# Kernel optimization log

Hardware: AMD Instinct MI355X
Metric: run time of the kernel (lower is better)

## Reference

```python
import jax, jax.numpy as jnp
import numpy as np

N_NODES = 100000
N_EDGES = 1600000
IN_DIM = 500
HID = 256
N_LAYERS = 3
N_CLASSES = 40


def setup_inputs() -> dict:
    key = jax.random.key(0)
    ks = jax.random.split(key, 16)
    x = jax.random.normal(ks[0], (N_NODES, IN_DIM), dtype=jnp.float32)
    edge_index = jax.random.randint(ks[1], (2, N_EDGES), 0, N_NODES, dtype=jnp.int64)
    s = 0.02
    embed_W = jax.random.normal(ks[2], (IN_DIM, HID), dtype=jnp.float32) * s
    embed_b = jnp.zeros((HID,), dtype=jnp.float32)
    conv_W = jax.random.normal(ks[3], (N_LAYERS, HID, HID), dtype=jnp.float32) * s
    conv_b = jnp.zeros((N_LAYERS, HID), dtype=jnp.float32)
    bn_gamma = jnp.ones((N_LAYERS, HID), dtype=jnp.float32)
    bn_beta = jnp.zeros((N_LAYERS, HID), dtype=jnp.float32)
    # classifier: 256 -> 128 -> 64 -> 32 -> 40
    cls_W0 = jax.random.normal(ks[4], (256, 128), dtype=jnp.float32) * s
    cls_b0 = jnp.zeros((128,), dtype=jnp.float32)
    cls_W1 = jax.random.normal(ks[5], (128, 64), dtype=jnp.float32) * s
    cls_b1 = jnp.zeros((64,), dtype=jnp.float32)
    cls_W2 = jax.random.normal(ks[6], (64, 32), dtype=jnp.float32) * s
    cls_b2 = jnp.zeros((32,), dtype=jnp.float32)
    cls_W3 = jax.random.normal(ks[7], (32, N_CLASSES), dtype=jnp.float32) * s
    cls_b3 = jnp.zeros((N_CLASSES,), dtype=jnp.float32)
    return dict(x=x, edge_index=edge_index, embed_W=embed_W, embed_b=embed_b,
                conv_W=conv_W, conv_b=conv_b, bn_gamma=bn_gamma, bn_beta=bn_beta,
                cls_W0=cls_W0, cls_b0=cls_b0, cls_W1=cls_W1, cls_b1=cls_b1,
                cls_W2=cls_W2, cls_b2=cls_b2, cls_W3=cls_W3, cls_b3=cls_b3)


def _gcn_forward(x, edge_index, embed_W, embed_b, conv_W, conv_b, bn_gamma, bn_beta,
                 cls_W0, cls_b0, cls_W1, cls_b1, cls_W2, cls_b2, cls_W3, cls_b3):
    src, dst = edge_index[0], edge_index[1]
    N = x.shape[0]
    # degree incl. self-loop (GCNConv add_self_loops=True)
    deg = jax.ops.segment_sum(jnp.ones_like(src, dtype=x.dtype), dst, num_segments=N) + 1.0
    dinv = jax.lax.rsqrt(deg)                       # [N]
    enorm = dinv[src] * dinv[dst]                   # [E] symmetric norm
    self_norm = (1.0 / deg)[:, None]                # [N,1] self-loop weight

    h = x @ embed_W + embed_b                       # embed; dropout is identity in eval
    for l in range(N_LAYERS):
        hw = h @ conv_W[l]                          # [N,HID] transform first
        msg = hw[src] * enorm[:, None]              # gather + normalize [E,HID]
        agg = jax.ops.segment_sum(msg, dst, num_segments=N) + hw * self_norm
        agg = agg + conv_b[l]
        hb = agg * bn_gamma[l] + bn_beta[l]         # BN eval mode (running mean 0, var 1)
        hb = jax.nn.relu(hb)
        h = hb + h                                  # residual (dims match)
    # classifier MLP
    h = jax.nn.relu(h @ cls_W0 + cls_b0)
    h = jax.nn.relu(h @ cls_W1 + cls_b1)
    h = jax.nn.relu(h @ cls_W2 + cls_b2)
    return h @ cls_W3 + cls_b3                      # logits [N, N_CLASSES]


def reference(x, edge_index, embed_W, embed_b, conv_W, conv_b, bn_gamma, bn_beta,
              cls_W0, cls_b0, cls_W1, cls_b1, cls_W2, cls_b2, cls_W3, cls_b3):
    return _gcn_forward(x, edge_index, embed_W, embed_b, conv_W, conv_b, bn_gamma, bn_beta,
                        cls_W0, cls_b0, cls_W1, cls_b1, cls_W2, cls_b2, cls_W3, cls_b3)
```

## Files before the change

kernel.cpp:

```cpp
#include <hip/hip_runtime.h>

#define N_NODES  100000
#define N_EDGES  1600000
#define IN_DIM   500
#define HID      256
#define N_LAYERS 3
#define N_CLASSES 40

typedef _Float16 f16;
typedef __attribute__((ext_vector_type(8))) _Float16 f16x8;
typedef __attribute__((ext_vector_type(4))) _Float16 f16x4;
typedef __attribute__((ext_vector_type(4))) float    f32x4;

template <int MODE>
__global__ __launch_bounds__(256) void mfma_gemm_kernel(
    const float* __restrict__ A, const f16* __restrict__ Bt,
    const float* __restrict__ bias, void* __restrict__ Cout,
    int M, int N, int K, int KP)
{
    __shared__ f16 Ah[128][32];
    __shared__ f16 Bs[128][32];

    const int tid  = threadIdx.x;
    const int lane = tid & 63;
    const int w    = tid >> 6;
    const int wr   = w >> 1;
    const int wc   = w & 1;
    const int m0   = blockIdx.x * 128;
    const int n0   = blockIdx.y * 128;

    const int srow = tid >> 2;
    const int sc8  = tid & 3;

    f32x4 acc[4][4];
    #pragma unroll
    for (int i = 0; i < 4; ++i)
        #pragma unroll
        for (int j = 0; j < 4; ++j)
            acc[i][j] = (f32x4){0.f, 0.f, 0.f, 0.f};

    for (int k0 = 0; k0 < KP; k0 += 32) {
        #pragma unroll
        for (int i = 0; i < 2; ++i) {
            const int r = srow + 64 * i;
            const int m = m0 + r;
            const int k = k0 + sc8 * 8;
            float4 lo = make_float4(0.f, 0.f, 0.f, 0.f);
            float4 hi = make_float4(0.f, 0.f, 0.f, 0.f);
            if (m < M) {
                if (k + 4 <= K) lo = *(const float4*)&A[(size_t)m * K + k];
                if (k + 8 <= K) hi = *(const float4*)&A[(size_t)m * K + k + 4];
            }
            f16x8 hv;
            hv[0] = (f16)lo.x; hv[1] = (f16)lo.y; hv[2] = (f16)lo.z; hv[3] = (f16)lo.w;
            hv[4] = (f16)hi.x; hv[5] = (f16)hi.y; hv[6] = (f16)hi.z; hv[7] = (f16)hi.w;
            *(f16x8*)&Ah[r][sc8 * 8] = hv;
        }
        #pragma unroll
        for (int i = 0; i < 2; ++i) {
            const int r = srow + 64 * i;
            *(f16x8*)&Bs[r][sc8 * 8] =
                *(const f16x8*)&Bt[(size_t)(n0 + r) * KP + k0 + sc8 * 8];
        }
        __syncthreads();

        const int fr = lane & 15;
        const int fg = (lane >> 4) * 8;
        f16x8 af[4], bf[4];
        #pragma unroll
        for (int i = 0; i < 4; ++i)
            af[i] = *(const f16x8*)&Ah[wr * 64 + i * 16 + fr][fg];
        #pragma unroll
        for (int j = 0; j < 4; ++j)
            bf[j] = *(const f16x8*)&Bs[wc * 64 + j * 16 + fr][fg];
        #pragma unroll
        for (int i = 0; i < 4; ++i)
            #pragma unroll
            for (int j = 0; j < 4; ++j)
                acc[i][j] = __builtin_amdgcn_mfma_f32_16x16x32_f16(
                    af[i], bf[j], acc[i][j], 0, 0, 0);
        __syncthreads();
    }

    const int fr = lane & 15;
    const int rg = (lane >> 4) * 4;
    #pragma unroll
    for (int i = 0; i < 4; ++i) {
        const int mrow = m0 + wr * 64 + i * 16 + rg;
        #pragma unroll
        for (int j = 0; j < 4; ++j) {
            const int col = n0 + wc * 64 + j * 16 + fr;
            const float b = (MODE == 0 || MODE == 1) ? bias[col] : 0.f;
            #pragma unroll
            for (int r = 0; r < 4; ++r) {
                const int m = mrow + r;
                if (m >= M) continue;
                float v = acc[i][j][r] + b;
                if (MODE == 1) v = fmaxf(v, 0.f);
                if (MODE == 4) ((f16*)Cout)[(size_t)m * N + col] = (f16)v;
                else           ((float*)Cout)[(size_t)m * N + col] = v;
            }
        }
    }
}

__global__ __launch_bounds__(256) void wt_kernel(
    const float* __restrict__ W, f16* __restrict__ Wt, int K, int N, int KP)
{
    const int i = blockIdx.x * 256 + threadIdx.x;
    if (i >= N * KP) return;
    const int n = i / KP;
    const int k = i - n * KP;
    Wt[i] = (k < K) ? (f16)W[(size_t)k * N + n] : (f16)0.f;
}

template <int MODE>
__global__ __launch_bounds__(256) void gemm_kernel(
    const float* __restrict__ A, const float* __restrict__ B,
    const float* __restrict__ bias, float* __restrict__ C,
    int M, int N, int K)
{
    __shared__ float As[16][68];
    __shared__ float Bsh[16][68];

    const int tid = threadIdx.x;
    const int tx = tid & 15;
    const int ty = tid >> 4;
    const int bm = blockIdx.x * 64;
    const int bn = blockIdx.y * 64;

    const int ar = tid >> 2;
    const int ac = (tid & 3) * 4;
    const int br = tid >> 4;
    const int bc = (tid & 15) * 4;

    float c[4][4] = {};

    for (int k0 = 0; k0 < K; k0 += 16) {
        {
            const int m = bm + ar;
            const int k = k0 + ac;
            float4 av = make_float4(0.f, 0.f, 0.f, 0.f);
            if (m < M && k < K) av = *(const float4*)&A[(size_t)m * K + k];
            As[ac + 0][ar] = av.x;
            As[ac + 1][ar] = av.y;
            As[ac + 2][ar] = av.z;
            As[ac + 3][ar] = av.w;
        }
        {
            const int k = k0 + br;
            const int n = bn + bc;
            float4 bv = make_float4(0.f, 0.f, 0.f, 0.f);
            if (k < K && n < N) bv = *(const float4*)&B[(size_t)k * N + n];
            Bsh[br][bc + 0] = bv.x;
            Bsh[br][bc + 1] = bv.y;
            Bsh[br][bc + 2] = bv.z;
            Bsh[br][bc + 3] = bv.w;
        }
        __syncthreads();

        #pragma unroll
        for (int kk = 0; kk < 16; ++kk) {
            const float4 av = *(const float4*)&As[kk][ty * 4];
            const float4 bv = *(const float4*)&Bsh[kk][tx * 4];
            const float a[4] = {av.x, av.y, av.z, av.w};
            const float b[4] = {bv.x, bv.y, bv.z, bv.w};
            #pragma unroll
            for (int i = 0; i < 4; ++i)
                #pragma unroll
                for (int j = 0; j < 4; ++j)
                    c[i][j] = fmaf(a[i], b[j], c[i][j]);
        }
        __syncthreads();
    }

    const int n = bn + tx * 4;
    if (n >= N) return;
    const float4 bias4 = *(const float4*)&bias[n];

    #pragma unroll
    for (int i = 0; i < 4; ++i) {
        const int m = bm + ty * 4 + i;
        if (m >= M) continue;
        float4 v = make_float4(c[i][0] + bias4.x, c[i][1] + bias4.y,
                               c[i][2] + bias4.z, c[i][3] + bias4.w);
        if (MODE == 1) {
            v.x = fmaxf(v.x, 0.f); v.y = fmaxf(v.y, 0.f);
            v.z = fmaxf(v.z, 0.f); v.w = fmaxf(v.w, 0.f);
        }
        *(float4*)&C[(size_t)m * N + n] = v;
    }
}

__global__ __launch_bounds__(256) void deg_kernel(
    const int* __restrict__ dst, int* __restrict__ deg)
{
    const int i = blockIdx.x * 256 + threadIdx.x;
    if (i < N_EDGES) atomicAdd(&deg[dst[i]], 1);
}

__global__ __launch_bounds__(256) void norm_kernel(
    const int* __restrict__ deg, float* __restrict__ dinv,
    float* __restrict__ selfnorm)
{
    const int i = blockIdx.x * 256 + threadIdx.x;
    if (i < N_NODES) {
        const float d = (float)deg[i] + 1.0f;
        dinv[i] = 1.0f / sqrtf(d);
        selfnorm[i] = 1.0f / d;
    }
}

__global__ __launch_bounds__(256) void scan1_kernel(
    const int* __restrict__ deg, int* __restrict__ offs,
    int* __restrict__ bsum, int n)
{
    __shared__ int tmp[256];
    const int i = blockIdx.x * 256 + threadIdx.x;
    const int v = (i < n) ? deg[i] : 0;
    tmp[threadIdx.x] = v;
    __syncthreads();
    #pragma unroll
    for (int off = 1; off < 256; off <<= 1) {
        const int t = (threadIdx.x >= off) ? tmp[threadIdx.x - off] : 0;
        __syncthreads();
        tmp[threadIdx.x] += t;
        __syncthreads();
    }
    const int inc = tmp[threadIdx.x];
    if (i < n) offs[i] = inc - v;
    if (threadIdx.x == 255) bsum[blockIdx.x] = inc;
}

__global__ __launch_bounds__(512) void scan2_kernel(int* __restrict__ bsum, int nb)
{
    __shared__ int tmp[512];
    const int i = threadIdx.x;
    const int v = (i < nb) ? bsum[i] : 0;
    tmp[i] = v;
    __syncthreads();
    #pragma unroll
    for (int off = 1; off < 512; off <<= 1) {
        const int t = (i >= off) ? tmp[i - off] : 0;
        __syncthreads();
        tmp[i] += t;
        __syncthreads();
    }
    if (i < nb) bsum[i] = tmp[i] - v;
}

__global__ __launch_bounds__(256) void scan3_kernel(
    int* __restrict__ offs, const int* __restrict__ bsum, int n)
{
    const int i = blockIdx.x * 256 + threadIdx.x;
    if (i < n) offs[i] += bsum[blockIdx.x];
}

__global__ __launch_bounds__(256) void fill_kernel(
    const int* __restrict__ src, const int* __restrict__ dst,
    const int* __restrict__ offs, int* __restrict__ fill,
    const float* __restrict__ dinv,
    int* __restrict__ csr_src, float* __restrict__ csr_w)
{
    const int e = blockIdx.x * 256 + threadIdx.x;
    if (e >= N_EDGES) return;
    const int s = src[e];
    const int d = dst[e];
    const int pos = offs[d] + atomicAdd(&fill[d], 1);
    csr_src[pos] = s;
    csr_w[pos] = dinv[s] * dinv[d];
}

__global__ __launch_bounds__(256) void gather_fused_kernel(
    const int* __restrict__ offs, const int* __restrict__ degi,
    const int* __restrict__ csr_src, const float* __restrict__ csr_w,
    const f16* __restrict__ hw, const float* __restrict__ snorm,
    const float* __restrict__ bias, const float* __restrict__ gamma,
    const float* __restrict__ beta, float* __restrict__ h)
{
    const int w = (blockIdx.x * 256 + threadIdx.x) >> 6;
    const int lane = threadIdx.x & 63;
    if (w >= N_NODES) return;
    const int start = offs[w];
    const int cnt = degi[w];
    const int col = lane * 4;

    float4 acc = make_float4(0.f, 0.f, 0.f, 0.f);
    int i = 0;
    for (; i + 2 <= cnt; i += 2) {
        const int   s0 = csr_src[start + i];
        const int   s1 = csr_src[start + i + 1];
        const float w0 = csr_w[start + i];
        const float w1 = csr_w[start + i + 1];
        const f16x4 v0 = *(const f16x4*)(hw + (size_t)s0 * HID + col);
        const f16x4 v1 = *(const f16x4*)(hw + (size_t)s1 * HID + col);
        acc.x = fmaf((float)v0[0], w0, acc.x); acc.y = fmaf((float)v0[1], w0, acc.y);
        acc.z = fmaf((float)v0[2], w0, acc.z); acc.w = fmaf((float)v0[3], w0, acc.w);
        acc.x = fmaf((float)v1[0], w1, acc.x); acc.y = fmaf((float)v1[1], w1, acc.y);
        acc.z = fmaf((float)v1[2], w1, acc.z); acc.w = fmaf((float)v1[3], w1, acc.w);
    }
    if (i < cnt) {
        const int   s0 = csr_src[start + i];
        const float w0 = csr_w[start + i];
        const f16x4 v0 = *(const f16x4*)(hw + (size_t)s0 * HID + col);
        acc.x = fmaf((float)v0[0], w0, acc.x); acc.y = fmaf((float)v0[1], w0, acc.y);
        acc.z = fmaf((float)v0[2], w0, acc.z); acc.w = fmaf((float)v0[3], w0, acc.w);
    }

    const float sn = snorm[w];
    const f16x4 hwv = *(const f16x4*)(hw + (size_t)w * HID + col);
    acc.x = fmaf((float)hwv[0], sn, acc.x); acc.y = fmaf((float)hwv[1], sn, acc.y);
    acc.z = fmaf((float)hwv[2], sn, acc.z); acc.w = fmaf((float)hwv[3], sn, acc.w);

    const float4 b4 = *(const float4*)&bias[col];
    const float4 g4 = *(const float4*)&gamma[col];
    const float4 t4 = *(const float4*)&beta[col];
    float* hp = h + (size_t)w * HID + col;
    float4 hv = *(float4*)hp;
    hv.x += fmaxf((acc.x + b4.x) * g4.x + t4.x, 0.f);
    hv.y += fmaxf((acc.y + b4.y) * g4.y + t4.y, 0.f);
    hv.z += fmaxf((acc.z + b4.z) * g4.z + t4.z, 0.f);
    hv.w += fmaxf((acc.w + b4.w) * g4.w + t4.w, 0.f);
    *(float4*)hp = hv;
}

extern "C" void kernel_launch(void* const* d_in, const int* in_sizes, int n_in,
                              void* d_out, int out_size, void* d_ws, size_t ws_size,
                              hipStream_t stream)
{
    const float* x        = (const float*)d_in[0];
    const int*   ei       = (const int*)d_in[1];
    const float* embed_W  = (const float*)d_in[2];
    const float* embed_b  = (const float*)d_in[3];
    const float* conv_W   = (const float*)d_in[4];
    const float* conv_b   = (const float*)d_in[5];
    const float* bn_gamma = (const float*)d_in[6];
    const float* bn_beta  = (const float*)d_in[7];
    const float* cls_W0   = (const float*)d_in[8];
    const float* cls_b0   = (const float*)d_in[9];
    const float* cls_W1   = (const float*)d_in[10];
    const float* cls_b1   = (const float*)d_in[11];
    const float* cls_W2   = (const float*)d_in[12];
    const float* cls_b2   = (const float*)d_in[13];
    const float* cls_W3   = (const float*)d_in[14];
    const float* cls_b3   = (const float*)d_in[15];
    float* out = (float*)d_out;

    const int* e_src = ei;
    const int* e_dst = ei + N_EDGES;

    char* p = (char*)d_ws;
    int*   deg_i   = (int*)p;                 p += (size_t)N_NODES * 4;
    int*   fillc   = (int*)p;                 p += (size_t)N_NODES * 4;
    int*   offs    = (int*)p;                 p += (size_t)N_NODES * 4;
    int*   bsum    = (int*)p;                 p += 512 * 4;
    float* dinv    = (float*)p;               p += (size_t)N_NODES * 4;
    float* snorm   = (float*)p;               p += (size_t)N_NODES * 4;
    int*   csr_src = (int*)p;                 p += (size_t)N_EDGES * 4;
    float* csr_w   = (float*)p;               p += (size_t)N_EDGES * 4;
    float* h       = (float*)p;               p += (size_t)N_NODES * HID * 4;
    f16*   hw16    = (f16*)p;                 p += (size_t)N_NODES * HID * 2;
    float* mlpA    = (float*)p;               p += (size_t)N_NODES * 128 * 4;
    float* mlpB    = (float*)p;               p += (size_t)N_NODES * 64 * 4;
    f16*   Wt_e    = (f16*)p;                 p += (size_t)256 * 512 * 2;
    f16*   Wt_c    = (f16*)p;                 p += (size_t)3 * 256 * 256 * 2;
    f16*   Wt_0    = (f16*)p;                 p += (size_t)128 * 256 * 2;

    const int NB_N = (N_NODES + 255) / 256;
    const int NB_E = (N_EDGES + 255) / 256;

    hipMemsetAsync(deg_i, 0, (size_t)2 * N_NODES * sizeof(int), stream);
    deg_kernel<<<NB_E, 256, 0, stream>>>(e_dst, deg_i);
    norm_kernel<<<NB_N, 256, 0, stream>>>(deg_i, dinv, snorm);
    scan1_kernel<<<NB_N, 256, 0, stream>>>(deg_i, offs, bsum, N_NODES);
    scan2_kernel<<<1, 512, 0, stream>>>(bsum, NB_N);
    scan3_kernel<<<NB_N, 256, 0, stream>>>(offs, bsum, N_NODES);
    fill_kernel<<<NB_E, 256, 0, stream>>>(e_src, e_dst, offs, fillc, dinv,
                                          csr_src, csr_w);

    wt_kernel<<<(256 * 512 + 255) / 256, 256, 0, stream>>>(embed_W, Wt_e, IN_DIM, HID, 512);
    for (int l = 0; l < N_LAYERS; ++l)
        wt_kernel<<<(256 * 256 + 255) / 256, 256, 0, stream>>>(
            conv_W + (size_t)l * HID * HID, Wt_c + (size_t)l * HID * HID, HID, HID, HID);
    wt_kernel<<<(128 * 256 + 255) / 256, 256, 0, stream>>>(cls_W0, Wt_0, 256, 128, 256);

    const int MB = (N_NODES + 127) / 128;
    const int MT = (N_NODES + 63) / 64;

    mfma_gemm_kernel<0><<<dim3(MB, 2), 256, 0, stream>>>(
        x, Wt_e, embed_b, h, N_NODES, HID, IN_DIM, 512);

    for (int l = 0; l < N_LAYERS; ++l) {
        mfma_gemm_kernel<4><<<dim3(MB, 2), 256, 0, stream>>>(
            h, Wt_c + (size_t)l * HID * HID, nullptr, hw16, N_NODES, HID, HID, HID);
        gather_fused_kernel<<<(N_NODES * 64 + 255) / 256, 256, 0, stream>>>(
            offs, deg_i, csr_src, csr_w, hw16, snorm,
            conv_b + l * HID, bn_gamma + l * HID, bn_beta + l * HID, h);
    }

    mfma_gemm_kernel<1><<<dim3(MB, 1), 256, 0, stream>>>(
        h, Wt_0, cls_b0, mlpA, N_NODES, 128, 256, 256);
    gemm_kernel<1><<<dim3(MT, 1), 256, 0, stream>>>(
        mlpA, cls_W1, cls_b1, mlpB, N_NODES, 64, 128);
    gemm_kernel<1><<<dim3(MT, 1), 256, 0, stream>>>(
        mlpB, cls_W2, cls_b2, mlpA, N_NODES, 32, 64);
    gemm_kernel<0><<<dim3(MT, 1), 256, 0, stream>>>(
        mlpA, cls_W3, cls_b3, out, N_NODES, N_CLASSES, 32);
}
```

Baseline: 1.306 ms.

## Keep an fp16 shadow of h and widen MFMA GEMM tiles with double buffering

The embedding GEMM and the gather kernel now also write an fp16 copy of the hidden state. The layer and classifier GEMMs read that fp16 copy instead of the fp32 h, which halves their A-operand traffic and removes the in-kernel conversion. The GEMM is generalised to a full-width N tile (256 columns with 512 threads), so A is read once per row block rather than twice, and it double-buffers LDS with register prefetch and padded rows. In exchange there are extra fp16 writes of h and a larger LDS and register footprint per block, which may lower occupancy.

```diff
diff --git a/kernel.cpp b/kernel.cpp
--- a/kernel.cpp
+++ b/kernel.cpp
@@ -12,25 +12,31 @@
 typedef __attribute__((ext_vector_type(4))) _Float16 f16x4;
 typedef __attribute__((ext_vector_type(4))) float    f32x4;
 
-template <int MODE>
-__global__ __launch_bounds__(256) void mfma_gemm_kernel(
-    const float* __restrict__ A, const f16* __restrict__ Bt,
+template <int MODE, int BN, bool AF16>
+__global__ __launch_bounds__(BN * 2) void mgemm_kernel(
+    const void* __restrict__ Ain, const f16* __restrict__ Bt,
     const float* __restrict__ bias, void* __restrict__ Cout,
-    int M, int N, int K, int KP)
-{
-    __shared__ f16 Ah[128][32];
-    __shared__ f16 Bs[128][32];
+    f16* __restrict__ C16, int M, int K, int KP)
+{
+    constexpr int T   = BN * 2;
+    constexpr int ACH = 256 / BN;
+    constexpr int RPC = T / 4;
+    constexpr int WC  = BN / 64;
+
+    __shared__ f16 Ah[2][128][40];
+    __shared__ f16 Bs[2][BN][40];
 
     const int tid  = threadIdx.x;
     const int lane = tid & 63;
-    const int w    = tid >> 6;
-    const int wr   = w >> 1;
-    const int wc   = w & 1;
+    const int wv   = tid >> 6;
+    const int wr   = wv / WC;
+    const int wc   = wv % WC;
     const int m0   = blockIdx.x * 128;
-    const int n0   = blockIdx.y * 128;
-
     const int srow = tid >> 2;
-    const int sc8  = tid & 3;
+    const int sc8  = (tid & 3) * 8;
+
+    const float* Af  = (const float*)Ain;
+    const f16*   A16 = (const f16*)Ain;
 
     f32x4 acc[4][4];
     #pragma unroll
@@ -39,40 +45,77 @@
         for (int j = 0; j < 4; ++j)
             acc[i][j] = (f32x4){0.f, 0.f, 0.f, 0.f};
 
-    for (int k0 = 0; k0 < KP; k0 += 32) {
+    float4 laL[ACH], laH[ACH];
+    f16x8  la16[ACH];
+    f16x8  lb[2];
+
+    const int nt = KP / 32;
+
+    auto load_regs = [&](int t) {
+        const int kb = t * 32 + sc8;
+        #pragma unroll
+        for (int i = 0; i < ACH; ++i) {
+            const int m = m0 + srow + i * RPC;
+            if (AF16) {
+                f16x8 v;
+                #pragma unroll
+                for (int q = 0; q < 8; ++q) v[q] = (f16)0.f;
+                if (m < M && kb + 8 <= K)
+                    v = *(const f16x8*)&A16[(size_t)m * K + kb];
+                la16[i] = v;
+            } else {
+                float4 lo = make_float4(0.f, 0.f, 0.f, 0.f);
+                float4 hi = make_float4(0.f, 0.f, 0.f, 0.f);
+                if (m < M) {
+                    if (kb + 4 <= K) lo = *(const float4*)&Af[(size_t)m * K + kb];
+                    if (kb + 8 <= K) hi = *(const float4*)&Af[(size_t)m * K + kb + 4];
+                }
+                laL[i] = lo; laH[i] = hi;
+            }
+        }
         #pragma unroll
         for (int i = 0; i < 2; ++i) {
-            const int r = srow + 64 * i;
-            const int m = m0 + r;
-            const int k = k0 + sc8 * 8;
-            float4 lo = make_float4(0.f, 0.f, 0.f, 0.f);
-            float4 hi = make_float4(0.f, 0.f, 0.f, 0.f);
-            if (m < M) {
-                if (k + 4 <= K) lo = *(const float4*)&A[(size_t)m * K + k];
-                if (k + 8 <= K) hi = *(const float4*)&A[(size_t)m * K + k + 4];
+            const int r = srow + i * RPC;
+            lb[i] = *(const f16x8*)&Bt[(size_t)r * KP + kb];
+        }
+    };
+
+    auto write_lds = [&](int buf) {
+        #pragma unroll
+        for (int i = 0; i < ACH; ++i) {
+            const int r = srow + i * RPC;
+            f16x8 hv;
+            if (AF16) {
+                hv = la16[i];
+            } else {
+                hv[0] = (f16)laL[i].x; hv[1] = (f16)laL[i].y;
+                hv[2] = (f16)laL[i].z; hv[3] = (f16)laL[i].w;
+                hv[4] = (f16)laH[i].x; hv[5] = (f16)laH[i].y;
+                hv[6] = (f16)laH[i].z; hv[7] = (f16)laH[i].w;
             }
-            f16x8 hv;
-            hv[0] = (f16)lo.x; hv[1] = (f16)lo.y; hv[2] = (f16)lo.z; hv[3] = (f16)lo.w;
-            hv[4] = (f16)hi.x; hv[5] = (f16)hi.y; hv[6] = (f16)hi.z; hv[7] = (f16)hi.w;
-            *(f16x8*)&Ah[r][sc8 * 8] = hv;
-        }
-        #pragma unroll
-        for (int i = 0; i < 2; ++i) {
-            const int r = srow + 64 * i;
-            *(f16x8*)&Bs[r][sc8 * 8] =
-                *(const f16x8*)&Bt[(size_t)(n0 + r) * KP + k0 + sc8 * 8];
-        }
-        __syncthreads();
-
+            *(f16x8*)&Ah[buf][r][sc8] = hv;
+        }
+        #pragma unroll
+        for (int i = 0; i < 2; ++i)
+            *(f16x8*)&Bs[buf][srow + i * RPC][sc8] = lb[i];
+    };
+
+    load_regs(0);
+    write_lds(0);
+    __syncthreads();
+
+    for (int t = 0; t < nt; ++t) {
+        if (t + 1 < nt) load_regs(t + 1);
+        const int buf = t & 1;
         const int fr = lane & 15;
         const int fg = (lane >> 4) * 8;
         f16x8 af[4], bf[4];
         #pragma unroll
         for (int i = 0; i < 4; ++i)
-            af[i] = *(const f16x8*)&Ah[wr * 64 + i * 16 + fr][fg];
+            af[i] = *(const f16x8*)&Ah[buf][wr * 64 + i * 16 + fr][fg];
         #pragma unroll
         for (int j = 0; j < 4; ++j)
-            bf[j] = *(const f16x8*)&Bs[wc * 64 + j * 16 + fr][fg];
+            bf[j] = *(const f16x8*)&Bs[buf][wc * 64 + j * 16 + fr][fg];
         #pragma unroll
         for (int i = 0; i < 4; ++i)
             #pragma unroll
@@ -80,25 +123,32 @@
                 acc[i][j] = __builtin_amdgcn_mfma_f32_16x16x32_f16(
                     af[i], bf[j], acc[i][j], 0, 0, 0);
         __syncthreads();
+        if (t + 1 < nt) {
+            write_lds((t + 1) & 1);
+            __syncthreads();
+        }
     }
 
     const int fr = lane & 15;
     const int rg = (lane >> 4) * 4;
     #pragma unroll
     for (int i = 0; i < 4; ++i) {
-        const int mrow = m0 + wr * 64 + i * 16 + rg;
         #pragma unroll
         for (int j = 0; j < 4; ++j) {
-            const int col = n0 + wc * 64 + j * 16 + fr;
+            const int col = wc * 64 + j * 16 + fr;
             const float b = (MODE == 0 || MODE == 1) ? bias[col] : 0.f;
             #pragma unroll
             for (int r = 0; r < 4; ++r) {
-                const int m = mrow + r;
+                const int m = m0 + wr * 64 + i * 16 + rg + r;
                 if (m >= M) continue;
                 float v = acc[i][j][r] + b;
                 if (MODE == 1) v = fmaxf(v, 0.f);
-                if (MODE == 4) ((f16*)Cout)[(size_t)m * N + col] = (f16)v;
-                else           ((float*)Cout)[(size_t)m * N + col] = v;
+                if (MODE == 4) {
+                    ((f16*)Cout)[(size_t)m * BN + col] = (f16)v;
+                } else {
+                    ((float*)Cout)[(size_t)m * BN + col] = v;
+                    if (MODE == 0) C16[(size_t)m * BN + col] = (f16)v;
+                }
             }
         }
     }
@@ -276,7 +326,8 @@
     const int* __restrict__ csr_src, const float* __restrict__ csr_w,
     const f16* __restrict__ hw, const float* __restrict__ snorm,
     const float* __restrict__ bias, const float* __restrict__ gamma,
-    const float* __restrict__ beta, float* __restrict__ h)
+    const float* __restrict__ beta, float* __restrict__ h,
+    f16* __restrict__ h16)
 {
     const int w = (blockIdx.x * 256 + threadIdx.x) >> 6;
     const int lane = threadIdx.x & 63;
@@ -322,6 +373,10 @@
     hv.z += fmaxf((acc.z + b4.z) * g4.z + t4.z, 0.f);
     hv.w += fmaxf((acc.w + b4.w) * g4.w + t4.w, 0.f);
     *(float4*)hp = hv;
+
+    f16x4 h4;
+    h4[0] = (f16)hv.x; h4[1] = (f16)hv.y; h4[2] = (f16)hv.z; h4[3] = (f16)hv.w;
+    *(f16x4*)(h16 + (size_t)w * HID + col) = h4;
 }
 
 extern "C" void kernel_launch(void* const* d_in, const int* in_sizes, int n_in,
@@ -359,6 +414,7 @@
     int*   csr_src = (int*)p;                 p += (size_t)N_EDGES * 4;
     float* csr_w   = (float*)p;               p += (size_t)N_EDGES * 4;
     float* h       = (float*)p;               p += (size_t)N_NODES * HID * 4;
+    f16*   h16     = (f16*)p;                 p += (size_t)N_NODES * HID * 2;
     f16*   hw16    = (f16*)p;                 p += (size_t)N_NODES * HID * 2;
     float* mlpA    = (float*)p;               p += (size_t)N_NODES * 128 * 4;
     float* mlpB    = (float*)p;               p += (size_t)N_NODES * 64 * 4;
@@ -387,19 +443,20 @@
     const int MB = (N_NODES + 127) / 128;
     const int MT = (N_NODES + 63) / 64;
 
-    mfma_gemm_kernel<0><<<dim3(MB, 2), 256, 0, stream>>>(
-        x, Wt_e, embed_b, h, N_NODES, HID, IN_DIM, 512);
+    mgemm_kernel<0, 256, false><<<MB, 512, 0, stream>>>(
+        x, Wt_e, embed_b, h, h16, N_NODES, IN_DIM, 512);
 
     for (int l = 0; l < N_LAYERS; ++l) {
-        mfma_gemm_kernel<4><<<dim3(MB, 2), 256, 0, stream>>>(
-            h, Wt_c + (size_t)l * HID * HID, nullptr, hw16, N_NODES, HID, HID, HID);
+        mgemm_kernel<4, 256, true><<<MB, 512, 0, stream>>>(
+            h16, Wt_c + (size_t)l * HID * HID, nullptr, hw16, nullptr,
+            N_NODES, HID, HID);
         gather_fused_kernel<<<(N_NODES * 64 + 255) / 256, 256, 0, stream>>>(
             offs, deg_i, csr_src, csr_w, hw16, snorm,
-            conv_b + l * HID, bn_gamma + l * HID, bn_beta + l * HID, h);
-    }
-
-    mfma_gemm_kernel<1><<<dim3(MB, 1), 256, 0, stream>>>(
-        h, Wt_0, cls_b0, mlpA, N_NODES, 128, 256, 256);
+            conv_b + l * HID, bn_gamma + l * HID, bn_beta + l * HID, h, h16);
+    }
+
+    mgemm_kernel<1, 128, true><<<MB, 256, 0, stream>>>(
+        h16, Wt_0, cls_b0, mlpA, nullptr, N_NODES, HID, HID);
     gemm_kernel<1><<<dim3(MT, 1), 256, 0, stream>>>(
         mlpA, cls_W1, cls_b1, mlpB, N_NODES, 64, 128);
     gemm_kernel<1><<<dim3(MT, 1), 256, 0, stream>>>(
```

New measurement: 1.218 ms. -6.7%, faster.
